# Kernel optimization log

Measured on AMD Instinct MI355X. Metric: run time of the kernel, lower is better.

The kernel has to match this reference:

```python
import jax, jax.numpy as jnp
import numpy as np

B, C, H, W, P_OUT = 8, 256, 96, 96, 256
EPS = 1e-5


def setup_inputs() -> dict:
    key = jax.random.key(0)
    k0, k1, k2 = jax.random.split(key, 3)
    x = jax.random.normal(k0, (B, C, H, W), jnp.float32)
    # ConvOffset2D weight: Conv2d(C, 2C, 3, padding=1, bias=False).
    # Original inits to zero; use small random weights for a non-trivial sampling pattern.
    w_off = jax.random.normal(k1, (2 * C, C, 3, 3), jnp.float32) * 0.01
    gamma = jnp.ones((C,), jnp.float32)
    beta = jnp.zeros((C,), jnp.float32)
    # pointwise Conv2d(C, P_OUT, 1, bias=False), kernel squeezed to (out, in)
    w_pw = jax.random.normal(k2, (P_OUT, C), jnp.float32) * (1.0 / np.sqrt(C))
    return {"x": x, "w_off": w_off, "gamma": gamma, "beta": beta, "w_pw": w_pw}


def _bilinear_sample(maps, coords):
    # maps: (N, Hm, Wm); coords: (N, P, 2) with [..., 0]=row(y), [..., 1]=col(x)
    N, Hm, Wm = maps.shape
    cy = jnp.clip(coords[..., 0], 0.0, Hm - 1)
    cx = jnp.clip(coords[..., 1], 0.0, Wm - 1)
    y0 = jnp.floor(cy)
    x0 = jnp.floor(cx)
    y0i = y0.astype(jnp.int32)
    x0i = x0.astype(jnp.int32)
    y1i = jnp.minimum(y0i + 1, Hm - 1)
    x1i = jnp.minimum(x0i + 1, Wm - 1)
    dy = cy - y0
    dx = cx - x0
    flat = maps.reshape(N, Hm * Wm)

    def g(yi, xi):
        return jnp.take_along_axis(flat, yi * Wm + xi, axis=1)

    v00 = g(y0i, x0i)
    v01 = g(y0i, x1i)
    v10 = g(y1i, x0i)
    v11 = g(y1i, x1i)
    top = v00 + (v01 - v00) * dx
    bot = v10 + (v11 - v10) * dx
    return top + (bot - top) * dy  # (N, P)


def reference(x, w_off, gamma, beta, w_pw):
    b, c, h, w = x.shape
    # fixed_padding(kernel=3, dilation=1) -> pad 1 on each side
    xp = jnp.pad(x, ((0, 0), (0, 0), (1, 1), (1, 1)))
    hp, wp = h + 2, w + 2
    # offset conv: (b, 2c, hp, wp)
    offsets = jax.lax.conv_general_dilated(
        xp, w_off, window_strides=(1, 1), padding=((1, 1), (1, 1)),
        dimension_numbers=("NCHW", "OIHW", "NCHW"))
    # original: view(-1, hp, wp, 2)  (flat-order reshape, channel pairs interleave over width)
    off = offsets.reshape(b * c, hp * wp, 2)
    gy, gx = jnp.meshgrid(jnp.arange(hp, dtype=jnp.float32),
                          jnp.arange(wp, dtype=jnp.float32), indexing="ij")
    grid = jnp.stack([gy.ravel(), gx.ravel()], axis=-1)  # (hp*wp, 2)
    coords = off + grid[None]
    sampled = _bilinear_sample(xp.reshape(b * c, hp, wp), coords)
    xd = sampled.reshape(b, c, hp, wp)[:, :, 1:-1, 1:-1]  # crop back to (h, w)
    # BatchNorm2d (training-mode batch statistics, biased var, eps=1e-5)
    mean = jnp.mean(xd, axis=(0, 2, 3), keepdims=True)
    var = jnp.var(xd, axis=(0, 2, 3), keepdims=True)
    xn = (xd - mean) * jax.lax.rsqrt(var + EPS)
    xn = xn * gamma[None, :, None, None] + beta[None, :, None, None]
    xr = jax.nn.relu(xn)
    # pointwise 1x1 conv
    return jnp.einsum("bchw,oc->bohw", xr, w_pw)
```

## Files before the change

kernel.cpp:

```cpp
#include <hip/hip_runtime.h>
#include <hip/hip_bf16.h>
#include <stdint.h>


#define BB 8
#define CI 256
#define HH 96
#define WW 96
#define WP 98
#define NSP 9604
#define NIN 9216
#define OC2 512

typedef __attribute__((ext_vector_type(8))) short short8;
typedef __attribute__((ext_vector_type(4))) float float4v;
typedef __attribute__((ext_vector_type(16))) float float16v;

__device__ __forceinline__ int bf16_mode(const void* gamma) {
  return *(const uint32_t*)gamma == 0x3F803F80u;
}
__device__ __forceinline__ float ldin(const void* p, long i, int bf) {
  return bf ? __bfloat162float(((const __hip_bfloat16*)p)[i])
            : ((const float*)p)[i];
}
__device__ __forceinline__ unsigned short f32_to_bf16_bits(float f) {
  uint32_t u = __float_as_uint(f);
  return (unsigned short)((u + 0x7FFFu + ((u >> 16) & 1u)) >> 16);
}
__device__ __forceinline__ float bf16_bits_to_f32(unsigned short b) {
  return __uint_as_float(((uint32_t)b) << 16);
}
__device__ __forceinline__ unsigned short ldbf(const void* p, long i, int bf) {
  if (bf) return ((const unsigned short*)p)[i];
  return f32_to_bf16_bits(((const float*)p)[i]);
}
__device__ __forceinline__ void gld16(const void* g, void* l) {
  __builtin_amdgcn_global_load_lds(
      (const __attribute__((address_space(1))) unsigned int*)g,
      (__attribute__((address_space(3))) unsigned int*)l, 16, 0, 0);
}

__global__ __launch_bounds__(256) void prep_kernel(
    const void* __restrict__ xin, const void* __restrict__ w_off,
    const void* __restrict__ w_pw, const void* __restrict__ gamma,
    unsigned short* __restrict__ Xp2, unsigned short* __restrict__ Wt,
    unsigned short* __restrict__ Wp) {
  const int bf = bf16_mode(gamma);
  if (blockIdx.x < 10000) {
    const int id = blockIdx.x * 256 + threadIdx.x;
    const int cc = id % 100;
    const int t1 = id / 100;
    const int rr = t1 % 100;
    const int bg = t1 / 100;
    const int y = rr - 2, x = cc - 2;
    const bool inb = ((unsigned)y < 96u) && ((unsigned)x < 96u);
    const long base = ((long)(bg * 8)) * (HH * WW) + (long)y * WW + x;
    short8 o;
#pragma unroll
    for (int j = 0; j < 8; ++j)
      o[j] = inb ? (short)ldbf(xin, base + (long)j * (HH * WW), bf) : (short)0;
    *(short8*)(Xp2 + (long)id * 8) = o;
  } else if (blockIdx.x < 10576) {
    const int id = (blockIdx.x - 10000) * 256 + threadIdx.x;
    const int oc = id & 511;
    const int tg = id >> 9;
    const int g = tg & 31, t = tg >> 5;
    short8 o;
#pragma unroll
    for (int j = 0; j < 8; ++j)
      o[j] = (short)ldbf(w_off, ((long)oc * CI + g * 8 + j) * 9 + t, bf);
    *(short8*)(Wt + (long)id * 8) = o;
  } else {
    const int id = (blockIdx.x - 10576) * 256 + threadIdx.x;
    const int oc = id & 255;
    const int g  = id >> 8;
    short8 o;
#pragma unroll
    for (int j = 0; j < 8; ++j)
      o[j] = (short)ldbf(w_pw, (long)oc * CI + g * 8 + j, bf);
    *(short8*)(Wp + (long)id * 8) = o;
  }
}

#define CONV_MFMA10                                                           \
    __builtin_amdgcn_s_setprio(1);                                            \
    acc[0][0] = __builtin_amdgcn_mfma_f32_32x32x16_bf16(af0, bv0, acc[0][0], 0, 0, 0); \
    acc[0][1] = __builtin_amdgcn_mfma_f32_32x32x16_bf16(af0, bv1, acc[0][1], 0, 0, 0); \
    acc[0][2] = __builtin_amdgcn_mfma_f32_32x32x16_bf16(af0, bv2, acc[0][2], 0, 0, 0); \
    acc[0][3] = __builtin_amdgcn_mfma_f32_32x32x16_bf16(af0, bv3, acc[0][3], 0, 0, 0); \
    acc[0][4] = __builtin_amdgcn_mfma_f32_32x32x16_bf16(af0, bv4, acc[0][4], 0, 0, 0); \
    acc[1][0] = __builtin_amdgcn_mfma_f32_32x32x16_bf16(af1, bv0, acc[1][0], 0, 0, 0); \
    acc[1][1] = __builtin_amdgcn_mfma_f32_32x32x16_bf16(af1, bv1, acc[1][1], 0, 0, 0); \
    acc[1][2] = __builtin_amdgcn_mfma_f32_32x32x16_bf16(af1, bv2, acc[1][2], 0, 0, 0); \
    acc[1][3] = __builtin_amdgcn_mfma_f32_32x32x16_bf16(af1, bv3, acc[1][3], 0, 0, 0); \
    acc[1][4] = __builtin_amdgcn_mfma_f32_32x32x16_bf16(af1, bv4, acc[1][4], 0, 0, 0); \
    __builtin_amdgcn_s_setprio(0);

#define CONV_FRAGS(KK)                                                        \
    short8 af0, af1, bv0, bv1, bv2, bv3, bv4;                                 \
    {                                                                         \
      const int kg = (KK) * 2 + lh;                                           \
      const unsigned short* ap = Ac + (kg * 256 + aRow) * 8;                  \
      af0 = *(const short8*)ap;                                               \
      af1 = *(const short8*)(ap + 256);                                       \
      const unsigned short* bp = Bc + (kg * 320 + bRow) * 8;                  \
      bv0 = *(const short8*)bp;                                               \
      bv1 = *(const short8*)(bp + 256);                                       \
      bv2 = *(const short8*)(bp + 512);                                       \
      bv3 = *(const short8*)(bp + 768);                                       \
      bv4 = *(const short8*)(bp + 1024);                                      \
    }

#define CONV_PHASE_WB(KK, PF, W)                                              \
  do {                                                                        \
    CONV_FRAGS(KK)                                                            \
    PF;                                                                       \
    asm volatile(W ::: "memory");                                             \
    __builtin_amdgcn_s_barrier();                                             \
    __builtin_amdgcn_sched_barrier(0);                                        \
    CONV_MFMA10                                                               \
  } while (0)

#define CONV_PHASE_NB(KK, PF)                                                 \
  do {                                                                        \
    CONV_FRAGS(KK)                                                            \
    PF;                                                                       \
    CONV_MFMA10                                                               \
  } while (0)

#define CONV_BAR2 { __builtin_amdgcn_s_barrier(); __builtin_amdgcn_sched_barrier(0); }

__global__ __launch_bounds__(512, 2) void conv_mfma(
    const unsigned short* __restrict__ Xp2, const unsigned short* __restrict__ Wt,
    unsigned short* __restrict__ offp) {
  extern __shared__ __align__(16) unsigned short lds[];
  unsigned short* As0 = lds;
  unsigned short* Bs0 = lds + 32768;

  const int tid = threadIdx.x;
  const int wv = tid >> 6, ln = tid & 63;
  const int lh = ln >> 5, lm = ln & 31;
  const int wm = wv >> 1, wn = wv & 1;
  const int b      = blockIdx.x;
  const int p_blk  = blockIdx.y * 320;
  const int oc_blk = blockIdx.z * 256;

  const int aRow = wm * 64 + lm;
  const int bRow = wn * 160 + lm;

  int aoffv[4], boff[5];
#pragma unroll
  for (int j = 0; j < 4; ++j) {
    int id = j * 512 + tid;
    aoffv[j] = ((id >> 8) * OC2 + oc_blk + (id & 255)) * 8;
  }
#pragma unroll
  for (int j = 0; j < 5; ++j) {
    int id = j * 512 + tid;
    int kg = id / 320, pl = id - kg * 320;
    int p = p_blk + pl;
    int r = p / WP; if (r > 97) r = 97;
    int c = p - r * WP; if (c > 97) c = 97;
    boff[j] = (kg * 10000 + r * 100 + c) * 8;
  }

  float16v acc[2][5];
#pragma unroll
  for (int m = 0; m < 2; ++m)
#pragma unroll
    for (int n = 0; n < 5; ++n)
#pragma unroll
      for (int r = 0; r < 16; ++r) acc[m][n][r] = 0.f;

  {
    const unsigned short* a2 = Wt;
    const unsigned short* b2 = Xp2 + (size_t)(b * 32) * 10000 * 8;
    gld16(a2 + aoffv[0], As0 + (0 * 512 + tid) * 8);
    gld16(b2 + boff[0], Bs0 + (0 * 512 + tid) * 8);
    gld16(b2 + boff[1], Bs0 + (1 * 512 + tid) * 8);
    gld16(a2 + aoffv[1], As0 + (1 * 512 + tid) * 8);
    gld16(b2 + boff[2], Bs0 + (2 * 512 + tid) * 8);
    gld16(a2 + aoffv[2], As0 + (2 * 512 + tid) * 8);
    gld16(b2 + boff[3], Bs0 + (3 * 512 + tid) * 8);
    gld16(a2 + aoffv[3], As0 + (3 * 512 + tid) * 8);
    gld16(b2 + boff[4], Bs0 + (4 * 512 + tid) * 8);
  }
  asm volatile("s_waitcnt vmcnt(6)" ::: "memory");
  __builtin_amdgcn_s_barrier();
  __builtin_amdgcn_sched_barrier(0);

  int t2 = 0, icb2 = 0;
  for (int s = 0; s < 35; ++s) {
    if (++t2 == 9) { t2 = 0; ++icb2; }
    const unsigned short* a2 = Wt + (size_t)(t2 * 32 + icb2 * 8) * (OC2 * 8);
    const unsigned short* b2 =
        Xp2 + ((size_t)(b * 32 + icb2 * 8) * 10000 + (t2 / 3) * 100 + (t2 % 3)) * 8;
    const unsigned short* Ac = As0 + (s & 1) * 16384;
    const unsigned short* Bc = Bs0 + (s & 1) * 20480;
    unsigned short* An = As0 + ((s & 1) ^ 1) * 16384;
    unsigned short* Bn = Bs0 + ((s & 1) ^ 1) * 20480;

    CONV_PHASE_WB(0,
        { gld16(a2 + aoffv[0], An + (0 * 512 + tid) * 8);
          gld16(b2 + boff[0], Bn + (0 * 512 + tid) * 8); },
        "s_waitcnt vmcnt(3)");
    CONV_PHASE_NB(1,
        { gld16(b2 + boff[1], Bn + (1 * 512 + tid) * 8);
          gld16(a2 + aoffv[1], An + (1 * 512 + tid) * 8); });
    CONV_PHASE_WB(2,
        { gld16(b2 + boff[2], Bn + (2 * 512 + tid) * 8);
          gld16(a2 + aoffv[2], An + (2 * 512 + tid) * 8); },
        "s_waitcnt vmcnt(3)");
    CONV_PHASE_NB(3,
        { gld16(b2 + boff[3], Bn + (3 * 512 + tid) * 8);
          gld16(a2 + aoffv[3], An + (3 * 512 + tid) * 8);
          gld16(b2 + boff[4], Bn + (4 * 512 + tid) * 8); });
    CONV_BAR2;
  }
  {
    const unsigned short* Ac = As0 + 16384;
    const unsigned short* Bc = Bs0 + 20480;
    CONV_PHASE_WB(0, {}, "s_waitcnt vmcnt(2)");
    CONV_PHASE_NB(1, {});
    CONV_PHASE_WB(2, {}, "s_waitcnt vmcnt(0)");
    CONV_PHASE_NB(3, {});
  }

#pragma unroll
  for (int n = 0; n < 5; ++n) {
    const int p = p_blk + wn * 160 + n * 32 + lm;
    if (p < NSP) {
#pragma unroll
      for (int m = 0; m < 2; ++m) {
        const int oc0 = oc_blk + wm * 64 + m * 32 + 4 * lh;
#pragma unroll
        for (int reg = 0; reg < 16; ++reg) {
          const int oc = oc0 + (reg & 3) + 8 * (reg >> 2);
          offp[((long)(b * OC2 + oc)) * NSP + p] = f32_to_bf16_bits(acc[m][n][reg]);
        }
      }
    }
  }
}

__global__ __launch_bounds__(256) void sample_kernel(
    const void* __restrict__ xin, const void* __restrict__ gamma,
    const unsigned short* __restrict__ offp,
    unsigned short* __restrict__ xd, float* __restrict__ partials) {
  const int bf  = bf16_mode(gamma);
  const int tid = threadIdx.x;
  const int n = blockIdx.x;
  const int b = n >> 8, c = n & 255;

  __shared__ __align__(16) unsigned short smap[9608];
  __shared__ float red[8];

  for (int i = tid; i < 1201; i += 256) ((short8*)smap)[i] = (short8)0;
  __syncthreads();
  const long xb = ((long)(b * CI + c)) * (HH * WW);
  for (int q = tid; q < 1152; q += 256) {
    int rr  = q / 12;
    int cc8 = (q - rr * 12) * 8;
    short8 v;
    if (bf) {
      v = *(const short8*)((const unsigned short*)xin + xb + rr * WW + cc8);
    } else {
#pragma unroll
      for (int k = 0; k < 8; ++k)
        v[k] = (short)f32_to_bf16_bits(((const float*)xin)[xb + rr * WW + cc8 + k]);
    }
    int basei = (rr + 1) * WP + 1 + cc8;
#pragma unroll
    for (int k = 0; k < 8; ++k) smap[basei + k] = (unsigned short)v[k];
  }
  __syncthreads();

  const long ob_even = ((long)(b * OC2 + 2 * c)) * NSP;
  const long ob_odd  = ob_even + NSP;
  float s1 = 0.f, s2 = 0.f;

  for (int it = 0; it < 36; ++it) {
    int i = tid + it * 256;
    int r  = 1 + i / WW;
    int cl = 1 + (i - (r - 1) * WW);
    int p  = r * WP + cl;
    long base = (p < 4802) ? (ob_even + 2 * p) : (ob_odd + 2 * (p - 4802));
    uint32_t pair = *(const uint32_t*)(offp + base);
    float offy = bf16_bits_to_f32((unsigned short)(pair & 0xffffu));
    float offx = bf16_bits_to_f32((unsigned short)(pair >> 16));
    float cy = fminf(fmaxf(offy + (float)r, 0.f), 97.f);
    float cx = fminf(fmaxf(offx + (float)cl, 0.f), 97.f);
    float y0 = floorf(cy), x0 = floorf(cx);
    int y0i = (int)y0, x0i = (int)x0;
    int y1i = y0i + 1 < 97 ? y0i + 1 : 97;
    int x1i = x0i + 1 < 97 ? x0i + 1 : 97;
    float dy = cy - y0, dx = cx - x0;
    float v00 = bf16_bits_to_f32(smap[y0i * WP + x0i]);
    float v01 = bf16_bits_to_f32(smap[y0i * WP + x1i]);
    float v10 = bf16_bits_to_f32(smap[y1i * WP + x0i]);
    float v11 = bf16_bits_to_f32(smap[y1i * WP + x1i]);
    float top = v00 + (v01 - v00) * dx;
    float bot = v10 + (v11 - v10) * dx;
    float val = top + (bot - top) * dy;
    unsigned short vb = f32_to_bf16_bits(val);
    float vr = bf16_bits_to_f32(vb);
    xd[(long)n * NIN + i] = vb;
    s1 += vr;
    s2 += vr * vr;
  }

#pragma unroll
  for (int o = 32; o > 0; o >>= 1) {
    s1 += __shfl_down(s1, o, 64);
    s2 += __shfl_down(s2, o, 64);
  }
  if ((tid & 63) == 0) { red[tid >> 6] = s1; red[4 + (tid >> 6)] = s2; }
  __syncthreads();
  if (tid == 0) {
    partials[n]        = red[0] + red[1] + red[2] + red[3];
    partials[2048 + n] = red[4] + red[5] + red[6] + red[7];
  }
}

__global__ __launch_bounds__(256) void bnrelu_t(
    const unsigned short* __restrict__ xd, const float* __restrict__ partials,
    const void* __restrict__ gamma, const void* __restrict__ beta,
    unsigned short* __restrict__ y) {
  const int bf = bf16_mode(gamma);
  const int tid = threadIdx.x;
  const int i0 = blockIdx.x * 64;
  const int b  = blockIdx.y;
  __shared__ unsigned short yt[64 * 256];

  float s1 = 0.f, s2 = 0.f;
#pragma unroll
  for (int bb = 0; bb < BB; ++bb) {
    s1 += partials[bb * 256 + tid];
    s2 += partials[2048 + bb * 256 + tid];
  }
  const float invn = 1.f / (float)(BB * NIN);
  float mean = s1 * invn;
  float var  = s2 * invn - mean * mean;
  float g  = ldin(gamma, tid, bf);
  float be = ldin(beta, tid, bf);
  float sc = g * rsqrtf(var + 1e-5f);
  float sh = be - mean * sc;

  const long xbase = ((long)(b * CI + tid)) * NIN + i0;
#pragma unroll
  for (int j = 0; j < 8; ++j) {
    short8 v = *(const short8*)(xd + xbase + j * 8);
#pragma unroll
    for (int k = 0; k < 8; ++k) {
      float f = bf16_bits_to_f32((unsigned short)v[k]);
      f = fmaxf(fmaf(f, sc, sh), 0.f);
      yt[(j * 8 + k) * 256 + tid] = f32_to_bf16_bits(f);
    }
  }
  __syncthreads();
  const int cb = (tid & 31) * 8;
  const int r0 = tid >> 5;
#pragma unroll
  for (int pass = 0; pass < 8; ++pass) {
    int ii = pass * 8 + r0;
    *(short8*)(y + ((long)(b * NIN + i0 + ii)) * CI + cb) =
        *(const short8*)&yt[ii * 256 + cb];
  }
}

__global__ __launch_bounds__(256) void pw_mfma(
    const unsigned short* __restrict__ y, const unsigned short* __restrict__ Wp,
    const void* __restrict__ gamma, void* __restrict__ out) {
  const int bfo = bf16_mode(gamma);
  __shared__ __align__(16) unsigned short As[8 * 128 * 8];
  __shared__ __align__(16) unsigned short Bs[8 * 128 * 8];
  const int tid = threadIdx.x;
  const int wv = tid >> 6, ln = tid & 63;
  const int b      = blockIdx.x;
  const int p_blk  = blockIdx.y * 128;
  const int oc_blk = blockIdx.z * 128;

  int aoffv[4], boffv[4];
  unsigned short* alds[4];
  unsigned short* blds[4];
#pragma unroll
  for (int i = 0; i < 4; ++i) {
    int id = tid + 256 * i;
    int gl = id >> 7, low = id & 127;
    aoffv[i] = (gl * 256 + oc_blk + low) * 8;
    boffv[i] = (p_blk + low) * CI + gl * 8;
    alds[i] = &As[id * 8];
    blds[i] = &Bs[id * 8];
  }
  const unsigned short* ybase = y + (long)b * NIN * CI;

  float4v acc[4][4];
#pragma unroll
  for (int m = 0; m < 4; ++m)
#pragma unroll
    for (int n = 0; n < 4; ++n) {
      acc[m][n][0] = 0.f; acc[m][n][1] = 0.f;
      acc[m][n][2] = 0.f; acc[m][n][3] = 0.f;
    }

  const int q = ln >> 4, col = ln & 15;
  const int ocw_l = (wv >> 1) * 64;
  const int pw_l  = (wv & 1) * 64;

  for (int ks = 0; ks < 4; ++ks) {
    const unsigned short* astep = Wp + ks * 16384;
    const unsigned short* bstep = ybase + ks * 64;
    __syncthreads();
#pragma unroll
    for (int i = 0; i < 4; ++i) {
      gld16(astep + aoffv[i], alds[i]);
      gld16(bstep + boffv[i], blds[i]);
    }
    __syncthreads();

#pragma unroll
    for (int kk = 0; kk < 2; ++kk) {
      const int qq = kk * 4 + q;
      short8 af[4], bfr[4];
#pragma unroll
      for (int m = 0; m < 4; ++m)
        af[m] = *(const short8*)&As[(qq * 128 + ocw_l + m * 16 + col) * 8];
#pragma unroll
      for (int n = 0; n < 4; ++n)
        bfr[n] = *(const short8*)&Bs[(qq * 128 + pw_l + n * 16 + col) * 8];
#pragma unroll
      for (int m = 0; m < 4; ++m)
#pragma unroll
        for (int n = 0; n < 4; ++n)
          acc[m][n] = __builtin_amdgcn_mfma_f32_16x16x32_bf16(
              af[m], bfr[n], acc[m][n], 0, 0, 0);
    }
  }

#pragma unroll
  for (int m = 0; m < 4; ++m) {
    const int oc = oc_blk + ocw_l + m * 16 + q * 4;
#pragma unroll
    for (int n = 0; n < 4; ++n) {
      const int p = p_blk + pw_l + n * 16 + col;
#pragma unroll
      for (int reg = 0; reg < 4; ++reg) {
        long idx = ((long)(b * CI + oc + reg)) * NIN + p;
        if (bfo) ((__hip_bfloat16*)out)[idx] = __float2bfloat16(acc[m][n][reg]);
        else ((float*)out)[idx] = acc[m][n][reg];
      }
    }
  }
}

extern "C" void kernel_launch(void* const* d_in, const int* in_sizes, int n_in,
                              void* d_out, int out_size, void* d_ws, size_t ws_size,
                              hipStream_t stream) {
  const void* x     = d_in[0];
  const void* w_off = d_in[1];
  const void* gamma = d_in[2];
  const void* beta  = d_in[3];
  const void* w_pw  = d_in[4];

  char*  ws   = (char*)d_ws;
  float* fws  = (float*)ws;
  char*  R1   = ws + 32768;
  unsigned short* Xp2 = (unsigned short*)R1;
  unsigned short* xd  = (unsigned short*)R1;
  unsigned short* yb  = (unsigned short*)(R1 + 37748736);
  unsigned short* Wt  = (unsigned short*)(R1 + 50331648);
  unsigned short* offp = (unsigned short*)(ws + 32768 + 75497472);
  unsigned short* Wp   = (unsigned short*)(ws + 32768 + 75497472 + 78675968);

  static int conv_lds_set = 0;
  if (!conv_lds_set) {
    (void)hipFuncSetAttribute((const void*)conv_mfma,
                              hipFuncAttributeMaxDynamicSharedMemorySize,
                              147456);
    conv_lds_set = 1;
  }

  prep_kernel<<<dim3(10608), 256, 0, stream>>>(x, w_off, w_pw, gamma, Xp2, Wt, Wp);
  conv_mfma<<<dim3(BB, 31, 2), dim3(512), 147456, stream>>>(Xp2, Wt, offp);
  sample_kernel<<<dim3(2048), 256, 0, stream>>>(x, gamma, offp, xd, fws);
  bnrelu_t<<<dim3(144, BB), 256, 0, stream>>>(xd, fws, gamma, beta, yb);
  pw_mfma<<<dim3(BB, 72, 2), 256, 0, stream>>>(yb, Wp, gamma, d_out);
}
```

Baseline: 404.6 us.

## Double-buffer MFMA register fragments to overlap LDS reads with MFMA

Restructures the offset-conv MFMA main loop so that LDS fragment reads for the next k-group go into a second register set (E/O ping-pong) while MFMAs consume the current set. Each phase now has a barrier plus waitcnt, and the next stage's first fragments are read before the loop iteration ends. The aim is to hide LDS read latency behind matrix instructions. In exchange it uses more VGPRs, which may pressure the 512-thread, 2-blocks-per-SM launch bound, and it adds barriers and more delicate vmcnt accounting.

```diff
diff --git a/kernel.cpp b/kernel.cpp
--- a/kernel.cpp
+++ b/kernel.cpp
@@ -82,53 +82,38 @@
   }
 }
 
-#define CONV_MFMA10                                                           \
-    __builtin_amdgcn_s_setprio(1);                                            \
-    acc[0][0] = __builtin_amdgcn_mfma_f32_32x32x16_bf16(af0, bv0, acc[0][0], 0, 0, 0); \
-    acc[0][1] = __builtin_amdgcn_mfma_f32_32x32x16_bf16(af0, bv1, acc[0][1], 0, 0, 0); \
-    acc[0][2] = __builtin_amdgcn_mfma_f32_32x32x16_bf16(af0, bv2, acc[0][2], 0, 0, 0); \
-    acc[0][3] = __builtin_amdgcn_mfma_f32_32x32x16_bf16(af0, bv3, acc[0][3], 0, 0, 0); \
-    acc[0][4] = __builtin_amdgcn_mfma_f32_32x32x16_bf16(af0, bv4, acc[0][4], 0, 0, 0); \
-    acc[1][0] = __builtin_amdgcn_mfma_f32_32x32x16_bf16(af1, bv0, acc[1][0], 0, 0, 0); \
-    acc[1][1] = __builtin_amdgcn_mfma_f32_32x32x16_bf16(af1, bv1, acc[1][1], 0, 0, 0); \
-    acc[1][2] = __builtin_amdgcn_mfma_f32_32x32x16_bf16(af1, bv2, acc[1][2], 0, 0, 0); \
-    acc[1][3] = __builtin_amdgcn_mfma_f32_32x32x16_bf16(af1, bv3, acc[1][3], 0, 0, 0); \
-    acc[1][4] = __builtin_amdgcn_mfma_f32_32x32x16_bf16(af1, bv4, acc[1][4], 0, 0, 0); \
-    __builtin_amdgcn_s_setprio(0);
-
-#define CONV_FRAGS(KK)                                                        \
-    short8 af0, af1, bv0, bv1, bv2, bv3, bv4;                                 \
-    {                                                                         \
-      const int kg = (KK) * 2 + lh;                                           \
-      const unsigned short* ap = Ac + (kg * 256 + aRow) * 8;                  \
-      af0 = *(const short8*)ap;                                               \
-      af1 = *(const short8*)(ap + 256);                                       \
-      const unsigned short* bp = Bc + (kg * 320 + bRow) * 8;                  \
-      bv0 = *(const short8*)bp;                                               \
-      bv1 = *(const short8*)(bp + 256);                                       \
-      bv2 = *(const short8*)(bp + 512);                                       \
-      bv3 = *(const short8*)(bp + 768);                                       \
-      bv4 = *(const short8*)(bp + 1024);                                      \
-    }
-
-#define CONV_PHASE_WB(KK, PF, W)                                              \
-  do {                                                                        \
-    CONV_FRAGS(KK)                                                            \
-    PF;                                                                       \
-    asm volatile(W ::: "memory");                                             \
-    __builtin_amdgcn_s_barrier();                                             \
-    __builtin_amdgcn_sched_barrier(0);                                        \
-    CONV_MFMA10                                                               \
-  } while (0)
-
-#define CONV_PHASE_NB(KK, PF)                                                 \
-  do {                                                                        \
-    CONV_FRAGS(KK)                                                            \
-    PF;                                                                       \
-    CONV_MFMA10                                                               \
-  } while (0)
-
-#define CONV_BAR2 { __builtin_amdgcn_s_barrier(); __builtin_amdgcn_sched_barrier(0); }
+#define FRAG_READ(SET, KG, AB, BB)                                            \
+  {                                                                           \
+    const unsigned short* ap_ = (AB) + ((KG) * 256 + aRow) * 8;               \
+    a##SET##0 = *(const short8*)ap_;                                          \
+    a##SET##1 = *(const short8*)(ap_ + 256);                                  \
+    const unsigned short* bp_ = (BB) + ((KG) * 320 + bRow) * 8;               \
+    b##SET##0 = *(const short8*)bp_;                                          \
+    b##SET##1 = *(const short8*)(bp_ + 256);                                  \
+    b##SET##2 = *(const short8*)(bp_ + 512);                                  \
+    b##SET##3 = *(const short8*)(bp_ + 768);                                  \
+    b##SET##4 = *(const short8*)(bp_ + 1024);                                 \
+  }
+
+#define MFMA10(SET)                                                           \
+  __builtin_amdgcn_s_setprio(1);                                              \
+  acc[0][0] = __builtin_amdgcn_mfma_f32_32x32x16_bf16(a##SET##0, b##SET##0, acc[0][0], 0, 0, 0); \
+  acc[0][1] = __builtin_amdgcn_mfma_f32_32x32x16_bf16(a##SET##0, b##SET##1, acc[0][1], 0, 0, 0); \
+  acc[0][2] = __builtin_amdgcn_mfma_f32_32x32x16_bf16(a##SET##0, b##SET##2, acc[0][2], 0, 0, 0); \
+  acc[0][3] = __builtin_amdgcn_mfma_f32_32x32x16_bf16(a##SET##0, b##SET##3, acc[0][3], 0, 0, 0); \
+  acc[0][4] = __builtin_amdgcn_mfma_f32_32x32x16_bf16(a##SET##0, b##SET##4, acc[0][4], 0, 0, 0); \
+  acc[1][0] = __builtin_amdgcn_mfma_f32_32x32x16_bf16(a##SET##1, b##SET##0, acc[1][0], 0, 0, 0); \
+  acc[1][1] = __builtin_amdgcn_mfma_f32_32x32x16_bf16(a##SET##1, b##SET##1, acc[1][1], 0, 0, 0); \
+  acc[1][2] = __builtin_amdgcn_mfma_f32_32x32x16_bf16(a##SET##1, b##SET##2, acc[1][2], 0, 0, 0); \
+  acc[1][3] = __builtin_amdgcn_mfma_f32_32x32x16_bf16(a##SET##1, b##SET##3, acc[1][3], 0, 0, 0); \
+  acc[1][4] = __builtin_amdgcn_mfma_f32_32x32x16_bf16(a##SET##1, b##SET##4, acc[1][4], 0, 0, 0); \
+  __builtin_amdgcn_s_setprio(0);                                              \
+  __builtin_amdgcn_sched_barrier(0);
+
+#define PH_SYNC(W)                                                            \
+  asm volatile(W ::: "memory");                                               \
+  __builtin_amdgcn_s_barrier();                                               \
+  __builtin_amdgcn_sched_barrier(0);
 
 __global__ __launch_bounds__(512, 2) void conv_mfma(
     const unsigned short* __restrict__ Xp2, const unsigned short* __restrict__ Wt,
@@ -171,6 +156,9 @@
     for (int n = 0; n < 5; ++n)
 #pragma unroll
       for (int r = 0; r < 16; ++r) acc[m][n][r] = 0.f;
+
+  short8 aE0, aE1, bE0, bE1, bE2, bE3, bE4;
+  short8 aO0, aO1, bO0, bO1, bO2, bO3, bO4;
 
   {
     const unsigned short* a2 = Wt;
@@ -185,9 +173,8 @@
     gld16(a2 + aoffv[3], As0 + (3 * 512 + tid) * 8);
     gld16(b2 + boff[4], Bs0 + (4 * 512 + tid) * 8);
   }
-  asm volatile("s_waitcnt vmcnt(6)" ::: "memory");
-  __builtin_amdgcn_s_barrier();
-  __builtin_amdgcn_sched_barrier(0);
+  PH_SYNC("s_waitcnt vmcnt(6)")
+  FRAG_READ(O, 0 + lh, As0, Bs0);
 
   int t2 = 0, icb2 = 0;
   for (int s = 0; s < 35; ++s) {
@@ -200,30 +187,51 @@
     unsigned short* An = As0 + ((s & 1) ^ 1) * 16384;
     unsigned short* Bn = Bs0 + ((s & 1) ^ 1) * 20480;
 
-    CONV_PHASE_WB(0,
-        { gld16(a2 + aoffv[0], An + (0 * 512 + tid) * 8);
-          gld16(b2 + boff[0], Bn + (0 * 512 + tid) * 8); },
-        "s_waitcnt vmcnt(3)");
-    CONV_PHASE_NB(1,
-        { gld16(b2 + boff[1], Bn + (1 * 512 + tid) * 8);
-          gld16(a2 + aoffv[1], An + (1 * 512 + tid) * 8); });
-    CONV_PHASE_WB(2,
-        { gld16(b2 + boff[2], Bn + (2 * 512 + tid) * 8);
-          gld16(a2 + aoffv[2], An + (2 * 512 + tid) * 8); },
-        "s_waitcnt vmcnt(3)");
-    CONV_PHASE_NB(3,
-        { gld16(b2 + boff[3], Bn + (3 * 512 + tid) * 8);
-          gld16(a2 + aoffv[3], An + (3 * 512 + tid) * 8);
-          gld16(b2 + boff[4], Bn + (4 * 512 + tid) * 8); });
-    CONV_BAR2;
+    PH_SYNC("s_waitcnt vmcnt(4)")
+    FRAG_READ(E, 2 + lh, Ac, Bc);
+    gld16(a2 + aoffv[0], An + (0 * 512 + tid) * 8);
+    gld16(b2 + boff[0], Bn + (0 * 512 + tid) * 8);
+    __builtin_amdgcn_sched_barrier(0);
+    MFMA10(O)
+
+    PH_SYNC("s_waitcnt vmcnt(4)")
+    FRAG_READ(O, 4 + lh, Ac, Bc);
+    gld16(b2 + boff[1], Bn + (1 * 512 + tid) * 8);
+    gld16(a2 + aoffv[1], An + (1 * 512 + tid) * 8);
+    __builtin_amdgcn_sched_barrier(0);
+    MFMA10(E)
+
+    PH_SYNC("s_waitcnt vmcnt(4)")
+    FRAG_READ(E, 6 + lh, Ac, Bc);
+    gld16(b2 + boff[2], Bn + (2 * 512 + tid) * 8);
+    gld16(a2 + aoffv[2], An + (2 * 512 + tid) * 8);
+    __builtin_amdgcn_sched_barrier(0);
+    MFMA10(O)
+
+    PH_SYNC("s_waitcnt vmcnt(3)")
+    FRAG_READ(O, 0 + lh, An, Bn);
+    gld16(b2 + boff[3], Bn + (3 * 512 + tid) * 8);
+    gld16(a2 + aoffv[3], An + (3 * 512 + tid) * 8);
+    gld16(b2 + boff[4], Bn + (4 * 512 + tid) * 8);
+    __builtin_amdgcn_sched_barrier(0);
+    MFMA10(E)
   }
   {
     const unsigned short* Ac = As0 + 16384;
     const unsigned short* Bc = Bs0 + 20480;
-    CONV_PHASE_WB(0, {}, "s_waitcnt vmcnt(2)");
-    CONV_PHASE_NB(1, {});
-    CONV_PHASE_WB(2, {}, "s_waitcnt vmcnt(0)");
-    CONV_PHASE_NB(3, {});
+    PH_SYNC("s_waitcnt vmcnt(4)")
+    FRAG_READ(E, 2 + lh, Ac, Bc);
+    __builtin_amdgcn_sched_barrier(0);
+    MFMA10(O)
+    PH_SYNC("s_waitcnt vmcnt(2)")
+    FRAG_READ(O, 4 + lh, Ac, Bc);
+    __builtin_amdgcn_sched_barrier(0);
+    MFMA10(E)
+    PH_SYNC("s_waitcnt vmcnt(0)")
+    FRAG_READ(E, 6 + lh, Ac, Bc);
+    __builtin_amdgcn_sched_barrier(0);
+    MFMA10(O)
+    MFMA10(E)
   }
 
 #pragma unroll
```

Result: slower. 419.0 us (+3.6%).
